# Performance work log

Hardware: AMD Instinct MI355X
Metric: run time of the kernel (lower is better)

## Reference

```python
import jax, jax.numpy as jnp
import numpy as np

HIDDEN = 256
ITEM_SIZE = 50000
SEQ_LEN = 256
BATCH = 256
ALPHA = 0.2      # LeakyReLU negative slope
LN_EPS = 1e-12


def setup_inputs() -> dict:
    key = jax.random.key(0)
    ks = jax.random.split(key, 8)
    item_seq = jax.random.randint(ks[0], (BATCH, SEQ_LEN), 0, ITEM_SIZE)
    item_emb_table = 0.02 * jax.random.normal(ks[1], (ITEM_SIZE, HIDDEN), dtype=jnp.float32)
    item_emb_table = item_emb_table.at[0].set(0.0)  # padding_idx=0
    pos_emb_table = 0.02 * jax.random.normal(ks[2], (SEQ_LEN, HIDDEN), dtype=jnp.float32)
    W = 0.02 * jax.random.normal(ks[3], (HIDDEN, HIDDEN), dtype=jnp.float32)  # stored [in,out]
    a1 = 0.02 * jax.random.normal(ks[4], (HIDDEN,), dtype=jnp.float32)  # a weight, first half (acts on h_i)
    a2 = 0.02 * jax.random.normal(ks[5], (HIDDEN,), dtype=jnp.float32)  # second half (acts on h_j)
    gamma = jnp.ones((HIDDEN,), dtype=jnp.float32)
    beta = jnp.zeros((HIDDEN,), dtype=jnp.float32)
    return {"item_seq": item_seq, "item_emb_table": item_emb_table,
            "pos_emb_table": pos_emb_table, "W": W, "a1": a1, "a2": a2,
            "gamma": gamma, "beta": beta}


def _layernorm(x, gamma, beta):
    mu = jnp.mean(x, axis=-1, keepdims=True)
    var = jnp.mean(jnp.square(x - mu), axis=-1, keepdims=True)
    return (x - mu) * jax.lax.rsqrt(var + LN_EPS) * gamma + beta


def reference(item_seq, item_emb_table, pos_emb_table, W, a1, a2, gamma, beta):
    B, L = item_seq.shape
    x = item_emb_table[item_seq] + pos_emb_table[jnp.arange(L)][None, :, :]  # [B,L,H]
    x = _layernorm(x, gamma, beta)
    # dropout is identity at eval time
    h = jnp.einsum('blh,hk->blk', x, W)  # GAT W projection, [B,L,H]
    # a([h_i ; h_j]) = a1.h_i + a2.h_j  -> rank-1 separable scores (same math, no O(L^2 H) concat)
    s1 = h @ a1  # [B,L]
    s2 = h @ a2  # [B,L]
    e = jax.nn.leaky_relu(s1[:, :, None] + s2[:, None, :], negative_slope=ALPHA)  # [B,L,L]
    # adj is all-ones, so the -9e15 mask is a no-op
    attn = jax.nn.softmax(e, axis=-1)
    return jnp.einsum('bij,bjh->bih', attn, h)  # [B,L,H]
```

## Files before the change

### kernel.cpp

```cpp
#include <hip/hip_runtime.h>
#include <hip/hip_bf16.h>

#define ALPHA  0.2f
#define L2E    1.4426950408889634f

typedef __attribute__((ext_vector_type(8))) short  short8;
typedef __attribute__((ext_vector_type(4))) float  f32x4;
typedef unsigned short u16;

__device__ __forceinline__ u16 f2bf(float f) {
    union { __hip_bfloat16 h; u16 u; } v;
    v.h = __float2bfloat16(f);
    return v.u;
}
__device__ __forceinline__ unsigned pk2(float a, float b) {
    union { __hip_bfloat162 h2; unsigned u; } v;
    float2 f2; f2.x = a; f2.y = b;
    v.h2 = __float22bfloat162_rn(f2);
    return v.u;
}
__device__ __forceinline__ float lrelu(float x) { return fmaxf(x, ALPHA * x); }

__global__ void prep(const float* __restrict__ W, const float* __restrict__ a1,
                     const float* __restrict__ a2, u16* __restrict__ wfrag,
                     float* __restrict__ w1, float* __restrict__ w2) {
    int b = blockIdx.x;
    if (b < 64) {
        int t    = threadIdx.x;
        int pair = b * 2 + (t >> 7);
        int l    = (t >> 1) & 63;
        int jh   = (t & 1) * 4;
        int ks   = pair >> 4, cb = pair & 15;
        int c  = cb * 16 + (l & 15);
        int k0 = ks * 32 + (l >> 4) * 8 + jh;
        ushort4 o;
        o.x = f2bf(W[(size_t)(k0 + 0) * 256 + c]);
        o.y = f2bf(W[(size_t)(k0 + 1) * 256 + c]);
        o.z = f2bf(W[(size_t)(k0 + 2) * 256 + c]);
        o.w = f2bf(W[(size_t)(k0 + 3) * 256 + c]);
        *(ushort4*)&wfrag[(size_t)pair * 512 + l * 8 + jh] = o;
    } else {
        int bb = b - 64;
        int wv = threadIdx.x >> 6, lane = threadIdx.x & 63;
        for (int kk = 0; kk < 16; ++kk) {
            int k = bb * 64 + wv * 16 + kk;
            float4 wv4 = *(const float4*)(W + (size_t)k * 256 + 4 * lane);
            float4 a14 = *(const float4*)(a1 + 4 * lane);
            float4 a24 = *(const float4*)(a2 + 4 * lane);
            float d1 = wv4.x*a14.x + wv4.y*a14.y + wv4.z*a14.z + wv4.w*a14.w;
            float d2 = wv4.x*a24.x + wv4.y*a24.y + wv4.z*a24.z + wv4.w*a24.w;
            #pragma unroll
            for (int off = 32; off; off >>= 1) {
                d1 += __shfl_xor(d1, off);
                d2 += __shfl_xor(d2, off);
            }
            if (lane == 0) { w1[k] = d1; w2[k] = d2; }
        }
    }
}

__global__ __launch_bounds__(1024)
void gat(const int* __restrict__ item_seq, const float* __restrict__ emb,
         const float* __restrict__ pos, const float* __restrict__ gamma,
         const float* __restrict__ beta, const float* __restrict__ w1,
         const float* __restrict__ w2, const u16* __restrict__ wfrag,
         float* __restrict__ out)
{
    __shared__ u16 xb[256 * 256];
    __shared__ __align__(16) float s1s[256], s2s[256], mS[256];
    __shared__ __align__(16) float part[256][4];
    __shared__ float wmax[16];
    const int b    = blockIdx.x;
    const int tid  = threadIdx.x;
    const int lane = tid & 63, wid = tid >> 6, g = lane >> 4, li = lane & 15;
    const int iw_  = wid >> 2, nw = wid & 3;

    {
        float4 g4  = *(const float4*)(gamma + 4 * lane);
        float4 b4  = *(const float4*)(beta  + 4 * lane);
        float4 w14 = *(const float4*)(w1    + 4 * lane);
        float4 w24 = *(const float4*)(w2    + 4 * lane);
        float4 u4, t4;
        u4.x = g4.x*w14.x; u4.y = g4.y*w14.y; u4.z = g4.z*w14.z; u4.w = g4.w*w14.w;
        t4.x = g4.x*w24.x; t4.y = g4.y*w24.y; t4.z = g4.z*w24.z; t4.w = g4.w*w24.w;
        float cA = u4.x + u4.y + u4.z + u4.w;
        float cB = t4.x + t4.y + t4.z + t4.w;
        float cC = b4.x*w14.x + b4.y*w14.y + b4.z*w14.z + b4.w*w14.w;
        float cD = b4.x*w24.x + b4.y*w24.y + b4.z*w24.z + b4.w*w24.w;
        #pragma unroll
        for (int off = 32; off; off >>= 1) {
            cA += __shfl_xor(cA, off); cB += __shfl_xor(cB, off);
            cC += __shfl_xor(cC, off); cD += __shfl_xor(cD, off);
        }
        float rm = -3.0e38f;
        #pragma unroll 2
        for (int it = 0; it < 8; ++it) {
            int rA = it * 32 + wid, rB = rA + 16;
            int gA = item_seq[b * 256 + rA];
            int gB = item_seq[b * 256 + rB];
            float4 eA = *(const float4*)(emb + (size_t)gA * 256 + 4 * lane);
            float4 pA = *(const float4*)(pos + (size_t)rA * 256 + 4 * lane);
            float4 eB = *(const float4*)(emb + (size_t)gB * 256 + 4 * lane);
            float4 pB = *(const float4*)(pos + (size_t)rB * 256 + 4 * lane);
            float4 vA, vB;
            vA.x = eA.x + pA.x; vA.y = eA.y + pA.y; vA.z = eA.z + pA.z; vA.w = eA.w + pA.w;
            vB.x = eB.x + pB.x; vB.y = eB.y + pB.y; vB.z = eB.z + pB.z; vB.w = eB.w + pB.w;
            float sa = vA.x + vA.y + vA.z + vA.w;
            float qa = vA.x*vA.x + vA.y*vA.y + vA.z*vA.z + vA.w*vA.w;
            float d1a = vA.x*u4.x + vA.y*u4.y + vA.z*u4.z + vA.w*u4.w;
            float d2a = vA.x*t4.x + vA.y*t4.y + vA.z*t4.z + vA.w*t4.w;
            float sb = vB.x + vB.y + vB.z + vB.w;
            float qb = vB.x*vB.x + vB.y*vB.y + vB.z*vB.z + vB.w*vB.w;
            float d1b = vB.x*u4.x + vB.y*u4.y + vB.z*u4.z + vB.w*u4.w;
            float d2b = vB.x*t4.x + vB.y*t4.y + vB.z*t4.z + vB.w*t4.w;
            #pragma unroll
            for (int off = 32; off; off >>= 1) {
                sa  += __shfl_xor(sa,  off);  sb  += __shfl_xor(sb,  off);
                qa  += __shfl_xor(qa,  off);  qb  += __shfl_xor(qb,  off);
                d1a += __shfl_xor(d1a, off);  d1b += __shfl_xor(d1b, off);
                d2a += __shfl_xor(d2a, off);  d2b += __shfl_xor(d2b, off);
            }
            float muA = sa * (1.0f/256.0f);
            float rsA = rsqrtf(qa * (1.0f/256.0f) - muA*muA + 1e-12f);
            float muB = sb * (1.0f/256.0f);
            float rsB = rsqrtf(qb * (1.0f/256.0f) - muB*muB + 1e-12f);
            float s1A = (rsA * (d1a - muA * cA) + cC) * L2E;
            float s2A = (rsA * (d2a - muA * cB) + cD) * L2E;
            float s1B = (rsB * (d1b - muB * cA) + cC) * L2E;
            float s2B = (rsB * (d2b - muB * cB) + cD) * L2E;
            if (lane == 0) {
                s1s[rA] = s1A; s2s[rA] = s2A;
                s1s[rB] = s1B; s2s[rB] = s2B;
            }
            rm = fmaxf(rm, fmaxf(s2A, s2B));
            uint2 oA, oB;
            oA.x = pk2((vA.x - muA) * rsA * g4.x + b4.x,
                       (vA.y - muA) * rsA * g4.y + b4.y);
            oA.y = pk2((vA.z - muA) * rsA * g4.z + b4.z,
                       (vA.w - muA) * rsA * g4.w + b4.w);
            oB.x = pk2((vB.x - muB) * rsB * g4.x + b4.x,
                       (vB.y - muB) * rsB * g4.y + b4.y);
            oB.y = pk2((vB.z - muB) * rsB * g4.z + b4.z,
                       (vB.w - muB) * rsB * g4.w + b4.w);
            int sl = (lane >> 1), sub = (lane & 1) * 4;
            *(uint2*)&xb[rA * 256 + ((sl ^ (rA & 7)) << 3) + sub] = oA;
            *(uint2*)&xb[rB * 256 + ((sl ^ (rB & 7)) << 3) + sub] = oB;
        }
        if (lane == 0) wmax[wid] = rm;
    }
    __syncthreads();

    {
        float s2m = wmax[0];
        #pragma unroll
        for (int k = 1; k < 16; ++k) s2m = fmaxf(s2m, wmax[k]);
        int i = tid >> 2, jq = tid & 3;
        float s1v = s1s[i];
        float mi  = lrelu(s1v + s2m);
        float aB0 = s1v - mi;
        float bB0 = ALPHA * s1v - mi;
        float sum = 0.f;
        const float4* sp = (const float4*)&s2s[jq * 64];
        #pragma unroll 4
        for (int j4 = 0; j4 < 16; ++j4) {
            float4 sv = sp[j4];
            sum += __builtin_amdgcn_exp2f(fmaxf(aB0 + sv.x, fmaf(ALPHA, sv.x, bB0)));
            sum += __builtin_amdgcn_exp2f(fmaxf(aB0 + sv.y, fmaf(ALPHA, sv.y, bB0)));
            sum += __builtin_amdgcn_exp2f(fmaxf(aB0 + sv.z, fmaf(ALPHA, sv.z, bB0)));
            sum += __builtin_amdgcn_exp2f(fmaxf(aB0 + sv.w, fmaf(ALPHA, sv.w, bB0)));
        }
        if (jq == 0) mS[i] = mi;
        part[i][jq] = sum;
    }

    f32x4 acc[4][4];
    #pragma unroll
    for (int mt = 0; mt < 4; ++mt)
        #pragma unroll
        for (int nt = 0; nt < 4; ++nt)
            acc[mt][nt] = (f32x4){0.f, 0.f, 0.f, 0.f};

    #pragma unroll
    for (int ks = 0; ks < 8; ++ks) {
        short8 bf[4];
        #pragma unroll
        for (int nt = 0; nt < 4; ++nt)
            bf[nt] = *(const short8*)(wfrag
                       + ((size_t)(ks * 16 + nw * 4 + nt) * 64 + lane) * 8);
        #pragma unroll
        for (int mt = 0; mt < 4; ++mt) {
            int rl = iw_ * 64 + mt * 16 + li;
            short8 af = *(const short8*)&xb[rl * 256 + (((ks*4+g) ^ (rl & 7)) << 3)];
            #pragma unroll
            for (int nt = 0; nt < 4; ++nt)
                acc[mt][nt] = __builtin_amdgcn_mfma_f32_16x16x32_bf16(
                    af, bf[nt], acc[mt][nt], 0, 0, 0);
        }
    }
    __syncthreads();

    #pragma unroll
    for (int mt = 0; mt < 4; ++mt)
        #pragma unroll
        for (int nt = 0; nt < 4; ++nt) {
            int c  = nw * 64 + nt * 16 + li;
            int i0 = iw_ * 64 + mt * 16 + 4 * g;
            uint2 o;
            o.x = pk2(acc[mt][nt][0], acc[mt][nt][1]);
            o.y = pk2(acc[mt][nt][2], acc[mt][nt][3]);
            *(uint2*)&xb[c * 256 + (((i0 >> 3) ^ (c & 7)) << 3) + (i0 & 7)] = o;
        }
    __syncthreads();

    {
        const int ig2 = wid >> 1;
        const int ng2 = wid & 1;
        f32x4 oacc[2][8];
        #pragma unroll
        for (int mt = 0; mt < 2; ++mt)
            #pragma unroll
            for (int nt = 0; nt < 8; ++nt)
                oacc[mt][nt] = (f32x4){0.f, 0.f, 0.f, 0.f};

        float aBase[2], bBase[2];
        #pragma unroll
        for (int mt = 0; mt < 2; ++mt) {
            int i = ig2 * 32 + mt * 16 + li;
            float lsum = part[i][0] + part[i][1] + part[i][2] + part[i][3];
            float Mi = mS[i] + __log2f(lsum);
            float s1v = s1s[i];
            aBase[mt] = s1v - Mi;
            bBase[mt] = ALPHA * s1v - Mi;
        }

        #pragma unroll
        for (int js = 0; js < 8; ++js) {
            float4 sv0 = *(const float4*)&s2s[js * 32 + g * 8];
            float4 sv1 = *(const float4*)&s2s[js * 32 + g * 8 + 4];
            float s2l[8] = {sv0.x, sv0.y, sv0.z, sv0.w, sv1.x, sv1.y, sv1.z, sv1.w};

            short8 pfr[2];
            #pragma unroll
            for (int mt = 0; mt < 2; ++mt) {
                union { unsigned int u[4]; short8 s; } pk;
                #pragma unroll
                for (int q2 = 0; q2 < 4; ++q2) {
                    float sA = s2l[2 * q2], sB = s2l[2 * q2 + 1];
                    float p0 = __builtin_amdgcn_exp2f(
                        fmaxf(aBase[mt] + sA, fmaf(ALPHA, sA, bBase[mt])));
                    float p1 = __builtin_amdgcn_exp2f(
                        fmaxf(aBase[mt] + sB, fmaf(ALPHA, sB, bBase[mt])));
                    pk.u[q2] = pk2(p0, p1);
                }
                pfr[mt] = pk.s;
            }
            #pragma unroll
            for (int nt = 0; nt < 8; ++nt) {
                int cl = ng2 * 128 + nt * 16 + li;
                short8 vf = *(const short8*)&xb[cl * 256
                              + (((js * 4 + g) ^ (cl & 7)) << 3)];
                #pragma unroll
                for (int mt = 0; mt < 2; ++mt)
                    oacc[mt][nt] = __builtin_amdgcn_mfma_f32_16x16x32_bf16(
                        pfr[mt], vf, oacc[mt][nt], 0, 0, 0);
            }
        }

        size_t ob = (size_t)b * (256 * 256);
        #pragma unroll
        for (int mt = 0; mt < 2; ++mt)
            #pragma unroll
            for (int nt = 0; nt < 8; ++nt) {
                int c  = ng2 * 128 + nt * 16 + li;
                int i0 = ig2 * 32 + mt * 16 + 4 * g;
                #pragma unroll
                for (int q2 = 0; q2 < 4; ++q2)
                    out[ob + (size_t)(i0 + q2) * 256 + c] = oacc[mt][nt][q2];
            }
    }
}

extern "C" void kernel_launch(void* const* d_in, const int* in_sizes, int n_in,
                              void* d_out, int out_size, void* d_ws, size_t ws_size,
                              hipStream_t stream) {
    (void)in_sizes; (void)n_in; (void)out_size; (void)ws_size;
    const int*   seq   = (const int*)d_in[0];
    const float* emb   = (const float*)d_in[1];
    const float* pos   = (const float*)d_in[2];
    const float* W     = (const float*)d_in[3];
    const float* a1    = (const float*)d_in[4];
    const float* a2    = (const float*)d_in[5];
    const float* gamma = (const float*)d_in[6];
    const float* beta  = (const float*)d_in[7];

    char* ws = (char*)d_ws;
    u16*   wfrag = (u16*)ws;
    float* w1    = (float*)(ws + 131072);
    float* w2    = (float*)(ws + 132096);

    hipLaunchKernelGGL(prep, dim3(68), dim3(256), 0, stream, W, a1, a2, wfrag, w1, w2);
    hipLaunchKernelGGL(gat, dim3(256), dim3(1024), 0, stream,
                       seq, emb, pos, gamma, beta, w1, w2, wfrag, (float*)d_out);
}
```

Baseline: 59.25 us.

## Fuse softmax denominator into PV pass and prefetch W fragments

Removes the separate softmax row-sum pass, which computed the exp sums up front, and instead accumulates row sums from the same exp values used to build the P fragments. The output is normalized at the end with a reciprocal gathered through shuffles. The LayerNorm load loop now handles four rows per iteration to raise memory-level parallelism, and the W fragment loads in the projection GEMM are software-prefetched one k-step ahead. The risk is that sums are taken in fp32 before bf16 rounding of P, so they differ slightly from the packed values, and that register pressure rises.

```diff
diff --git a/kernel.cpp b/kernel.cpp
--- a/kernel.cpp
+++ b/kernel.cpp
@@ -67,9 +67,9 @@
          float* __restrict__ out)
 {
     __shared__ u16 xb[256 * 256];
-    __shared__ __align__(16) float s1s[256], s2s[256], mS[256];
-    __shared__ __align__(16) float part[256][4];
+    __shared__ __align__(16) float s1s[256], s2s[256];
     __shared__ float wmax[16];
+    __shared__ float s2r;
     const int b    = blockIdx.x;
     const int tid  = threadIdx.x;
     const int lane = tid & 63, wid = tid >> 6, g = lane >> 4, li = lane & 15;
@@ -93,84 +93,67 @@
             cC += __shfl_xor(cC, off); cD += __shfl_xor(cD, off);
         }
         float rm = -3.0e38f;
-        #pragma unroll 2
-        for (int it = 0; it < 8; ++it) {
-            int rA = it * 32 + wid, rB = rA + 16;
-            int gA = item_seq[b * 256 + rA];
-            int gB = item_seq[b * 256 + rB];
-            float4 eA = *(const float4*)(emb + (size_t)gA * 256 + 4 * lane);
-            float4 pA = *(const float4*)(pos + (size_t)rA * 256 + 4 * lane);
-            float4 eB = *(const float4*)(emb + (size_t)gB * 256 + 4 * lane);
-            float4 pB = *(const float4*)(pos + (size_t)rB * 256 + 4 * lane);
-            float4 vA, vB;
-            vA.x = eA.x + pA.x; vA.y = eA.y + pA.y; vA.z = eA.z + pA.z; vA.w = eA.w + pA.w;
-            vB.x = eB.x + pB.x; vB.y = eB.y + pB.y; vB.z = eB.z + pB.z; vB.w = eB.w + pB.w;
-            float sa = vA.x + vA.y + vA.z + vA.w;
-            float qa = vA.x*vA.x + vA.y*vA.y + vA.z*vA.z + vA.w*vA.w;
-            float d1a = vA.x*u4.x + vA.y*u4.y + vA.z*u4.z + vA.w*u4.w;
-            float d2a = vA.x*t4.x + vA.y*t4.y + vA.z*t4.z + vA.w*t4.w;
-            float sb = vB.x + vB.y + vB.z + vB.w;
-            float qb = vB.x*vB.x + vB.y*vB.y + vB.z*vB.z + vB.w*vB.w;
-            float d1b = vB.x*u4.x + vB.y*u4.y + vB.z*u4.z + vB.w*u4.w;
-            float d2b = vB.x*t4.x + vB.y*t4.y + vB.z*t4.z + vB.w*t4.w;
+        for (int it = 0; it < 4; ++it) {
+            int r0 = it * 64 + wid;
+            int gI[4];
+            #pragma unroll
+            for (int m = 0; m < 4; ++m) gI[m] = item_seq[b * 256 + r0 + m * 16];
+            float4 e[4], p[4];
+            #pragma unroll
+            for (int m = 0; m < 4; ++m)
+                e[m] = *(const float4*)(emb + (size_t)gI[m] * 256 + 4 * lane);
+            #pragma unroll
+            for (int m = 0; m < 4; ++m)
+                p[m] = *(const float4*)(pos + (size_t)(r0 + m * 16) * 256 + 4 * lane);
+            float4 v[4]; float s[4], q[4], d1[4], d2[4];
+            #pragma unroll
+            for (int m = 0; m < 4; ++m) {
+                float4 vv;
+                vv.x = e[m].x + p[m].x; vv.y = e[m].y + p[m].y;
+                vv.z = e[m].z + p[m].z; vv.w = e[m].w + p[m].w;
+                v[m] = vv;
+                s[m]  = vv.x + vv.y + vv.z + vv.w;
+                q[m]  = vv.x*vv.x + vv.y*vv.y + vv.z*vv.z + vv.w*vv.w;
+                d1[m] = vv.x*u4.x + vv.y*u4.y + vv.z*u4.z + vv.w*u4.w;
+                d2[m] = vv.x*t4.x + vv.y*t4.y + vv.z*t4.z + vv.w*t4.w;
+            }
             #pragma unroll
             for (int off = 32; off; off >>= 1) {
-                sa  += __shfl_xor(sa,  off);  sb  += __shfl_xor(sb,  off);
-                qa  += __shfl_xor(qa,  off);  qb  += __shfl_xor(qb,  off);
-                d1a += __shfl_xor(d1a, off);  d1b += __shfl_xor(d1b, off);
-                d2a += __shfl_xor(d2a, off);  d2b += __shfl_xor(d2b, off);
-            }
-            float muA = sa * (1.0f/256.0f);
-            float rsA = rsqrtf(qa * (1.0f/256.0f) - muA*muA + 1e-12f);
-            float muB = sb * (1.0f/256.0f);
-            float rsB = rsqrtf(qb * (1.0f/256.0f) - muB*muB + 1e-12f);
-            float s1A = (rsA * (d1a - muA * cA) + cC) * L2E;
-            float s2A = (rsA * (d2a - muA * cB) + cD) * L2E;
-            float s1B = (rsB * (d1b - muB * cA) + cC) * L2E;
-            float s2B = (rsB * (d2b - muB * cB) + cD) * L2E;
-            if (lane == 0) {
-                s1s[rA] = s1A; s2s[rA] = s2A;
-                s1s[rB] = s1B; s2s[rB] = s2B;
-            }
-            rm = fmaxf(rm, fmaxf(s2A, s2B));
-            uint2 oA, oB;
-            oA.x = pk2((vA.x - muA) * rsA * g4.x + b4.x,
-                       (vA.y - muA) * rsA * g4.y + b4.y);
-            oA.y = pk2((vA.z - muA) * rsA * g4.z + b4.z,
-                       (vA.w - muA) * rsA * g4.w + b4.w);
-            oB.x = pk2((vB.x - muB) * rsB * g4.x + b4.x,
-                       (vB.y - muB) * rsB * g4.y + b4.y);
-            oB.y = pk2((vB.z - muB) * rsB * g4.z + b4.z,
-                       (vB.w - muB) * rsB * g4.w + b4.w);
-            int sl = (lane >> 1), sub = (lane & 1) * 4;
-            *(uint2*)&xb[rA * 256 + ((sl ^ (rA & 7)) << 3) + sub] = oA;
-            *(uint2*)&xb[rB * 256 + ((sl ^ (rB & 7)) << 3) + sub] = oB;
+                #pragma unroll
+                for (int m = 0; m < 4; ++m) {
+                    s[m]  += __shfl_xor(s[m],  off);
+                    q[m]  += __shfl_xor(q[m],  off);
+                    d1[m] += __shfl_xor(d1[m], off);
+                    d2[m] += __shfl_xor(d2[m], off);
+                }
+            }
+            #pragma unroll
+            for (int m = 0; m < 4; ++m) {
+                int r = r0 + m * 16;
+                float mu  = s[m] * (1.0f/256.0f);
+                float rs  = rsqrtf(q[m] * (1.0f/256.0f) - mu*mu + 1e-12f);
+                float s1v = (rs * (d1[m] - mu * cA) + cC) * L2E;
+                float s2v = (rs * (d2[m] - mu * cB) + cD) * L2E;
+                if (lane == 0) { s1s[r] = s1v; s2s[r] = s2v; }
+                rm = fmaxf(rm, s2v);
+                uint2 o;
+                o.x = pk2((v[m].x - mu) * rs * g4.x + b4.x,
+                          (v[m].y - mu) * rs * g4.y + b4.y);
+                o.y = pk2((v[m].z - mu) * rs * g4.z + b4.z,
+                          (v[m].w - mu) * rs * g4.w + b4.w);
+                int sl = (lane >> 1), sub = (lane & 1) * 4;
+                *(uint2*)&xb[r * 256 + ((sl ^ (r & 7)) << 3) + sub] = o;
+            }
         }
         if (lane == 0) wmax[wid] = rm;
     }
     __syncthreads();
 
-    {
-        float s2m = wmax[0];
-        #pragma unroll
-        for (int k = 1; k < 16; ++k) s2m = fmaxf(s2m, wmax[k]);
-        int i = tid >> 2, jq = tid & 3;
-        float s1v = s1s[i];
-        float mi  = lrelu(s1v + s2m);
-        float aB0 = s1v - mi;
-        float bB0 = ALPHA * s1v - mi;
-        float sum = 0.f;
-        const float4* sp = (const float4*)&s2s[jq * 64];
-        #pragma unroll 4
-        for (int j4 = 0; j4 < 16; ++j4) {
-            float4 sv = sp[j4];
-            sum += __builtin_amdgcn_exp2f(fmaxf(aB0 + sv.x, fmaf(ALPHA, sv.x, bB0)));
-            sum += __builtin_amdgcn_exp2f(fmaxf(aB0 + sv.y, fmaf(ALPHA, sv.y, bB0)));
-            sum += __builtin_amdgcn_exp2f(fmaxf(aB0 + sv.z, fmaf(ALPHA, sv.z, bB0)));
-            sum += __builtin_amdgcn_exp2f(fmaxf(aB0 + sv.w, fmaf(ALPHA, sv.w, bB0)));
-        }
-        if (jq == 0) mS[i] = mi;
-        part[i][jq] = sum;
+    if (tid == 0) {
+        float m0 = wmax[0];
+        #pragma unroll
+        for (int k = 1; k < 16; ++k) m0 = fmaxf(m0, wmax[k]);
+        s2r = m0;
     }
 
     f32x4 acc[4][4];
@@ -180,21 +163,34 @@
         for (int nt = 0; nt < 4; ++nt)
             acc[mt][nt] = (f32x4){0.f, 0.f, 0.f, 0.f};
 
-    #pragma unroll
-    for (int ks = 0; ks < 8; ++ks) {
+    {
         short8 bf[4];
         #pragma unroll
         for (int nt = 0; nt < 4; ++nt)
             bf[nt] = *(const short8*)(wfrag
-                       + ((size_t)(ks * 16 + nw * 4 + nt) * 64 + lane) * 8);
-        #pragma unroll
-        for (int mt = 0; mt < 4; ++mt) {
-            int rl = iw_ * 64 + mt * 16 + li;
-            short8 af = *(const short8*)&xb[rl * 256 + (((ks*4+g) ^ (rl & 7)) << 3)];
-            #pragma unroll
-            for (int nt = 0; nt < 4; ++nt)
-                acc[mt][nt] = __builtin_amdgcn_mfma_f32_16x16x32_bf16(
-                    af, bf[nt], acc[mt][nt], 0, 0, 0);
+                       + ((size_t)(nw * 4 + nt) * 64 + lane) * 8);
+        #pragma unroll
+        for (int ks = 0; ks < 8; ++ks) {
+            short8 bfn[4];
+            if (ks < 7) {
+                #pragma unroll
+                for (int nt = 0; nt < 4; ++nt)
+                    bfn[nt] = *(const short8*)(wfrag
+                               + ((size_t)((ks + 1) * 16 + nw * 4 + nt) * 64 + lane) * 8);
+            }
+            #pragma unroll
+            for (int mt = 0; mt < 4; ++mt) {
+                int rl = iw_ * 64 + mt * 16 + li;
+                short8 af = *(const short8*)&xb[rl * 256 + (((ks*4+g) ^ (rl & 7)) << 3)];
+                #pragma unroll
+                for (int nt = 0; nt < 4; ++nt)
+                    acc[mt][nt] = __builtin_amdgcn_mfma_f32_16x16x32_bf16(
+                        af, bf[nt], acc[mt][nt], 0, 0, 0);
+            }
+            if (ks < 7) {
+                #pragma unroll
+                for (int nt = 0; nt < 4; ++nt) bf[nt] = bfn[nt];
+            }
         }
     }
     __syncthreads();
@@ -222,15 +218,16 @@
             for (int nt = 0; nt < 8; ++nt)
                 oacc[mt][nt] = (f32x4){0.f, 0.f, 0.f, 0.f};
 
-        float aBase[2], bBase[2];
+        float s2m = s2r;
+        float aBase[2], bBase[2], pl[2];
         #pragma unroll
         for (int mt = 0; mt < 2; ++mt) {
             int i = ig2 * 32 + mt * 16 + li;
-            float lsum = part[i][0] + part[i][1] + part[i][2] + part[i][3];
-            float Mi = mS[i] + __log2f(lsum);
             float s1v = s1s[i];
-            aBase[mt] = s1v - Mi;
-            bBase[mt] = ALPHA * s1v - Mi;
+            float mi  = lrelu(s1v + s2m);
+            aBase[mt] = s1v - mi;
+            bBase[mt] = fmaf(ALPHA, s1v, -mi);
+            pl[mt] = 0.f;
         }
 
         #pragma unroll
@@ -250,6 +247,7 @@
                         fmaxf(aBase[mt] + sA, fmaf(ALPHA, sA, bBase[mt])));
                     float p1 = __builtin_amdgcn_exp2f(
                         fmaxf(aBase[mt] + sB, fmaf(ALPHA, sB, bBase[mt])));
+                    pl[mt] += p0 + p1;
                     pk.u[q2] = pk2(p0, p1);
                 }
                 pfr[mt] = pk.s;
@@ -266,6 +264,17 @@
             }
         }
 
+        float linv[2][4];
+        #pragma unroll
+        for (int mt = 0; mt < 2; ++mt) {
+            float t = pl[mt];
+            t += __shfl_xor(t, 16);
+            t += __shfl_xor(t, 32);
+            #pragma unroll
+            for (int q2 = 0; q2 < 4; ++q2)
+                linv[mt][q2] = 1.0f / __shfl(t, 4 * g + q2);
+        }
+
         size_t ob = (size_t)b * (256 * 256);
         #pragma unroll
         for (int mt = 0; mt < 2; ++mt)
@@ -275,7 +284,7 @@
                 int i0 = ig2 * 32 + mt * 16 + 4 * g;
                 #pragma unroll
                 for (int q2 = 0; q2 < 4; ++q2)
-                    out[ob + (size_t)(i0 + q2) * 256 + c] = oacc[mt][nt][q2];
+                    out[ob + (size_t)(i0 + q2) * 256 + c] = oacc[mt][nt][q2] * linv[mt][q2];
             }
     }
 }
```

Measured after the change: 59.91 us. Within noise of the previous version (+1.1%).

## Split LN+projection into halves and fold softmax normalization into epilogue

Applied to the files above, without the earlier changes.

The embedding, LayerNorm and projection work is split into two 128-row halves. Gathers for the second half are issued early and the first-half MFMA projection runs while that second half is being prepared, which is meant to hide gather latency behind tensor-core work. The separate softmax row-sum pass (with its part/mS shared arrays and log) is removed. Row sums are instead accumulated during the P computation, and the output is scaled by their reciprocal in the epilogue. The wave tiling of the projection also changes from 4x4 to 2x8. The trade-off is more live registers (eU, acc0, acc1), which raises spill or pressure risk at 1024 threads.

```diff
diff --git a/kernel.cpp b/kernel.cpp
--- a/kernel.cpp
+++ b/kernel.cpp
@@ -67,152 +67,220 @@
          float* __restrict__ out)
 {
     __shared__ u16 xb[256 * 256];
-    __shared__ __align__(16) float s1s[256], s2s[256], mS[256];
-    __shared__ __align__(16) float part[256][4];
+    __shared__ __align__(16) float s1s[256], s2s[256];
     __shared__ float wmax[16];
     const int b    = blockIdx.x;
     const int tid  = threadIdx.x;
     const int lane = tid & 63, wid = tid >> 6, g = lane >> 4, li = lane & 15;
-    const int iw_  = wid >> 2, nw = wid & 3;
-
-    {
-        float4 g4  = *(const float4*)(gamma + 4 * lane);
-        float4 b4  = *(const float4*)(beta  + 4 * lane);
-        float4 w14 = *(const float4*)(w1    + 4 * lane);
-        float4 w24 = *(const float4*)(w2    + 4 * lane);
-        float4 u4, t4;
-        u4.x = g4.x*w14.x; u4.y = g4.y*w14.y; u4.z = g4.z*w14.z; u4.w = g4.w*w14.w;
-        t4.x = g4.x*w24.x; t4.y = g4.y*w24.y; t4.z = g4.z*w24.z; t4.w = g4.w*w24.w;
-        float cA = u4.x + u4.y + u4.z + u4.w;
-        float cB = t4.x + t4.y + t4.z + t4.w;
-        float cC = b4.x*w14.x + b4.y*w14.y + b4.z*w14.z + b4.w*w14.w;
-        float cD = b4.x*w24.x + b4.y*w24.y + b4.z*w24.z + b4.w*w24.w;
+    const int iw2  = wid >> 3, nw8 = wid & 7;
+
+    float4 g4  = *(const float4*)(gamma + 4 * lane);
+    float4 b4  = *(const float4*)(beta  + 4 * lane);
+    float4 w14 = *(const float4*)(w1    + 4 * lane);
+    float4 w24 = *(const float4*)(w2    + 4 * lane);
+    float4 u4, t4;
+    u4.x = g4.x*w14.x; u4.y = g4.y*w14.y; u4.z = g4.z*w14.z; u4.w = g4.w*w14.w;
+    t4.x = g4.x*w24.x; t4.y = g4.y*w24.y; t4.z = g4.z*w24.z; t4.w = g4.w*w24.w;
+    float cA = u4.x + u4.y + u4.z + u4.w;
+    float cB = t4.x + t4.y + t4.z + t4.w;
+    float cC = b4.x*w14.x + b4.y*w14.y + b4.z*w14.z + b4.w*w14.w;
+    float cD = b4.x*w24.x + b4.y*w24.y + b4.z*w24.z + b4.w*w24.w;
+    #pragma unroll
+    for (int off = 32; off; off >>= 1) {
+        cA += __shfl_xor(cA, off); cB += __shfl_xor(cB, off);
+        cC += __shfl_xor(cC, off); cD += __shfl_xor(cD, off);
+    }
+
+    int gU[8];
+    #pragma unroll
+    for (int m = 0; m < 8; ++m) gU[m] = item_seq[b * 256 + 128 + m * 16 + wid];
+
+    float rm = -3.0e38f;
+
+    #pragma unroll 2
+    for (int it = 0; it < 4; ++it) {
+        int rA = it * 32 + wid, rB = rA + 16;
+        int gA = item_seq[b * 256 + rA];
+        int gB = item_seq[b * 256 + rB];
+        float4 eA = *(const float4*)(emb + (size_t)gA * 256 + 4 * lane);
+        float4 pA = *(const float4*)(pos + (size_t)rA * 256 + 4 * lane);
+        float4 eB = *(const float4*)(emb + (size_t)gB * 256 + 4 * lane);
+        float4 pB = *(const float4*)(pos + (size_t)rB * 256 + 4 * lane);
+        float4 vA, vB;
+        vA.x = eA.x + pA.x; vA.y = eA.y + pA.y; vA.z = eA.z + pA.z; vA.w = eA.w + pA.w;
+        vB.x = eB.x + pB.x; vB.y = eB.y + pB.y; vB.z = eB.z + pB.z; vB.w = eB.w + pB.w;
+        float sa = vA.x + vA.y + vA.z + vA.w;
+        float qa = vA.x*vA.x + vA.y*vA.y + vA.z*vA.z + vA.w*vA.w;
+        float d1a = vA.x*u4.x + vA.y*u4.y + vA.z*u4.z + vA.w*u4.w;
+        float d2a = vA.x*t4.x + vA.y*t4.y + vA.z*t4.z + vA.w*t4.w;
+        float sb = vB.x + vB.y + vB.z + vB.w;
+        float qb = vB.x*vB.x + vB.y*vB.y + vB.z*vB.z + vB.w*vB.w;
+        float d1b = vB.x*u4.x + vB.y*u4.y + vB.z*u4.z + vB.w*u4.w;
+        float d2b = vB.x*t4.x + vB.y*t4.y + vB.z*t4.z + vB.w*t4.w;
         #pragma unroll
         for (int off = 32; off; off >>= 1) {
-            cA += __shfl_xor(cA, off); cB += __shfl_xor(cB, off);
-            cC += __shfl_xor(cC, off); cD += __shfl_xor(cD, off);
-        }
-        float rm = -3.0e38f;
-        #pragma unroll 2
-        for (int it = 0; it < 8; ++it) {
-            int rA = it * 32 + wid, rB = rA + 16;
-            int gA = item_seq[b * 256 + rA];
-            int gB = item_seq[b * 256 + rB];
-            float4 eA = *(const float4*)(emb + (size_t)gA * 256 + 4 * lane);
-            float4 pA = *(const float4*)(pos + (size_t)rA * 256 + 4 * lane);
-            float4 eB = *(const float4*)(emb + (size_t)gB * 256 + 4 * lane);
-            float4 pB = *(const float4*)(pos + (size_t)rB * 256 + 4 * lane);
-            float4 vA, vB;
-            vA.x = eA.x + pA.x; vA.y = eA.y + pA.y; vA.z = eA.z + pA.z; vA.w = eA.w + pA.w;
-            vB.x = eB.x + pB.x; vB.y = eB.y + pB.y; vB.z = eB.z + pB.z; vB.w = eB.w + pB.w;
-            float sa = vA.x + vA.y + vA.z + vA.w;
-            float qa = vA.x*vA.x + vA.y*vA.y + vA.z*vA.z + vA.w*vA.w;
-            float d1a = vA.x*u4.x + vA.y*u4.y + vA.z*u4.z + vA.w*u4.w;
-            float d2a = vA.x*t4.x + vA.y*t4.y + vA.z*t4.z + vA.w*t4.w;
-            float sb = vB.x + vB.y + vB.z + vB.w;
-            float qb = vB.x*vB.x + vB.y*vB.y + vB.z*vB.z + vB.w*vB.w;
-            float d1b = vB.x*u4.x + vB.y*u4.y + vB.z*u4.z + vB.w*u4.w;
-            float d2b = vB.x*t4.x + vB.y*t4.y + vB.z*t4.z + vB.w*t4.w;
-            #pragma unroll
-            for (int off = 32; off; off >>= 1) {
-                sa  += __shfl_xor(sa,  off);  sb  += __shfl_xor(sb,  off);
-                qa  += __shfl_xor(qa,  off);  qb  += __shfl_xor(qb,  off);
-                d1a += __shfl_xor(d1a, off);  d1b += __shfl_xor(d1b, off);
-                d2a += __shfl_xor(d2a, off);  d2b += __shfl_xor(d2b, off);
-            }
-            float muA = sa * (1.0f/256.0f);
-            float rsA = rsqrtf(qa * (1.0f/256.0f) - muA*muA + 1e-12f);
-            float muB = sb * (1.0f/256.0f);
-            float rsB = rsqrtf(qb * (1.0f/256.0f) - muB*muB + 1e-12f);
-            float s1A = (rsA * (d1a - muA * cA) + cC) * L2E;
-            float s2A = (rsA * (d2a - muA * cB) + cD) * L2E;
-            float s1B = (rsB * (d1b - muB * cA) + cC) * L2E;
-            float s2B = (rsB * (d2b - muB * cB) + cD) * L2E;
-            if (lane == 0) {
-                s1s[rA] = s1A; s2s[rA] = s2A;
-                s1s[rB] = s1B; s2s[rB] = s2B;
-            }
-            rm = fmaxf(rm, fmaxf(s2A, s2B));
-            uint2 oA, oB;
-            oA.x = pk2((vA.x - muA) * rsA * g4.x + b4.x,
-                       (vA.y - muA) * rsA * g4.y + b4.y);
-            oA.y = pk2((vA.z - muA) * rsA * g4.z + b4.z,
-                       (vA.w - muA) * rsA * g4.w + b4.w);
-            oB.x = pk2((vB.x - muB) * rsB * g4.x + b4.x,
-                       (vB.y - muB) * rsB * g4.y + b4.y);
-            oB.y = pk2((vB.z - muB) * rsB * g4.z + b4.z,
-                       (vB.w - muB) * rsB * g4.w + b4.w);
-            int sl = (lane >> 1), sub = (lane & 1) * 4;
-            *(uint2*)&xb[rA * 256 + ((sl ^ (rA & 7)) << 3) + sub] = oA;
-            *(uint2*)&xb[rB * 256 + ((sl ^ (rB & 7)) << 3) + sub] = oB;
-        }
-        if (lane == 0) wmax[wid] = rm;
-    }
+            sa  += __shfl_xor(sa,  off);  sb  += __shfl_xor(sb,  off);
+            qa  += __shfl_xor(qa,  off);  qb  += __shfl_xor(qb,  off);
+            d1a += __shfl_xor(d1a, off);  d1b += __shfl_xor(d1b, off);
+            d2a += __shfl_xor(d2a, off);  d2b += __shfl_xor(d2b, off);
+        }
+        float muA = sa * (1.0f/256.0f);
+        float rsA = rsqrtf(qa * (1.0f/256.0f) - muA*muA + 1e-12f);
+        float muB = sb * (1.0f/256.0f);
+        float rsB = rsqrtf(qb * (1.0f/256.0f) - muB*muB + 1e-12f);
+        float s1A = (rsA * (d1a - muA * cA) + cC) * L2E;
+        float s2A = (rsA * (d2a - muA * cB) + cD) * L2E;
+        float s1B = (rsB * (d1b - muB * cA) + cC) * L2E;
+        float s2B = (rsB * (d2b - muB * cB) + cD) * L2E;
+        if (lane == 0) {
+            s1s[rA] = s1A; s2s[rA] = s2A;
+            s1s[rB] = s1B; s2s[rB] = s2B;
+        }
+        rm = fmaxf(rm, fmaxf(s2A, s2B));
+        uint2 oA, oB;
+        oA.x = pk2((vA.x - muA) * rsA * g4.x + b4.x,
+                   (vA.y - muA) * rsA * g4.y + b4.y);
+        oA.y = pk2((vA.z - muA) * rsA * g4.z + b4.z,
+                   (vA.w - muA) * rsA * g4.w + b4.w);
+        oB.x = pk2((vB.x - muB) * rsB * g4.x + b4.x,
+                   (vB.y - muB) * rsB * g4.y + b4.y);
+        oB.y = pk2((vB.z - muB) * rsB * g4.z + b4.z,
+                   (vB.w - muB) * rsB * g4.w + b4.w);
+        int sl = (lane >> 1), sub = (lane & 1) * 4;
+        *(uint2*)&xb[rA * 256 + ((sl ^ (rA & 7)) << 3) + sub] = oA;
+        *(uint2*)&xb[rB * 256 + ((sl ^ (rB & 7)) << 3) + sub] = oB;
+    }
+    __syncthreads();
+
+    float4 eU[8];
+    #pragma unroll
+    for (int m = 0; m < 8; ++m)
+        eU[m] = *(const float4*)(emb + (size_t)gU[m] * 256 + 4 * lane);
+
+    f32x4 acc0[4][2];
+    #pragma unroll
+    for (int mt = 0; mt < 4; ++mt)
+        #pragma unroll
+        for (int nt = 0; nt < 2; ++nt)
+            acc0[mt][nt] = (f32x4){0.f, 0.f, 0.f, 0.f};
+    #pragma unroll
+    for (int ks = 0; ks < 8; ++ks) {
+        short8 bf[2];
+        #pragma unroll
+        for (int nt = 0; nt < 2; ++nt)
+            bf[nt] = *(const short8*)(wfrag
+                       + ((size_t)(ks * 16 + nw8 * 2 + nt) * 64 + lane) * 8);
+        #pragma unroll
+        for (int mt = 0; mt < 4; ++mt) {
+            int rl = iw2 * 64 + mt * 16 + li;
+            short8 af = *(const short8*)&xb[rl * 256 + (((ks*4+g) ^ (rl & 7)) << 3)];
+            #pragma unroll
+            for (int nt = 0; nt < 2; ++nt)
+                acc0[mt][nt] = __builtin_amdgcn_mfma_f32_16x16x32_bf16(
+                    af, bf[nt], acc0[mt][nt], 0, 0, 0);
+        }
+    }
+
+    #pragma unroll 2
+    for (int it = 0; it < 4; ++it) {
+        int rA = 128 + it * 32 + wid, rB = rA + 16;
+        float4 eA = eU[2 * it], eB = eU[2 * it + 1];
+        float4 pA = *(const float4*)(pos + (size_t)rA * 256 + 4 * lane);
+        float4 pB = *(const float4*)(pos + (size_t)rB * 256 + 4 * lane);
+        float4 vA, vB;
+        vA.x = eA.x + pA.x; vA.y = eA.y + pA.y; vA.z = eA.z + pA.z; vA.w = eA.w + pA.w;
+        vB.x = eB.x + pB.x; vB.y = eB.y + pB.y; vB.z = eB.z + pB.z; vB.w = eB.w + pB.w;
+        float sa = vA.x + vA.y + vA.z + vA.w;
+        float qa = vA.x*vA.x + vA.y*vA.y + vA.z*vA.z + vA.w*vA.w;
+        float d1a = vA.x*u4.x + vA.y*u4.y + vA.z*u4.z + vA.w*u4.w;
+        float d2a = vA.x*t4.x + vA.y*t4.y + vA.z*t4.z + vA.w*t4.w;
+        float sb = vB.x + vB.y + vB.z + vB.w;
+        float qb = vB.x*vB.x + vB.y*vB.y + vB.z*vB.z + vB.w*vB.w;
+        float d1b = vB.x*u4.x + vB.y*u4.y + vB.z*u4.z + vB.w*u4.w;
+        float d2b = vB.x*t4.x + vB.y*t4.y + vB.z*t4.z + vB.w*t4.w;
+        #pragma unroll
+        for (int off = 32; off; off >>= 1) {
+            sa  += __shfl_xor(sa,  off);  sb  += __shfl_xor(sb,  off);
+            qa  += __shfl_xor(qa,  off);  qb  += __shfl_xor(qb,  off);
+            d1a += __shfl_xor(d1a, off);  d1b += __shfl_xor(d1b, off);
+            d2a += __shfl_xor(d2a, off);  d2b += __shfl_xor(d2b, off);
+        }
+        float muA = sa * (1.0f/256.0f);
+        float rsA = rsqrtf(qa * (1.0f/256.0f) - muA*muA + 1e-12f);
+        float muB = sb * (1.0f/256.0f);
+        float rsB = rsqrtf(qb * (1.0f/256.0f) - muB*muB + 1e-12f);
+        float s1A = (rsA * (d1a - muA * cA) + cC) * L2E;
+        float s2A = (rsA * (d2a - muA * cB) + cD) * L2E;
+        float s1B = (rsB * (d1b - muB * cA) + cC) * L2E;
+        float s2B = (rsB * (d2b - muB * cB) + cD) * L2E;
+        if (lane == 0) {
+            s1s[rA] = s1A; s2s[rA] = s2A;
+            s1s[rB] = s1B; s2s[rB] = s2B;
+        }
+        rm = fmaxf(rm, fmaxf(s2A, s2B));
+        uint2 oA, oB;
+        oA.x = pk2((vA.x - muA) * rsA * g4.x + b4.x,
+                   (vA.y - muA) * rsA * g4.y + b4.y);
+        oA.y = pk2((vA.z - muA) * rsA * g4.z + b4.z,
+                   (vA.w - muA) * rsA * g4.w + b4.w);
+        oB.x = pk2((vB.x - muB) * rsB * g4.x + b4.x,
+                   (vB.y - muB) * rsB * g4.y + b4.y);
+        oB.y = pk2((vB.z - muB) * rsB * g4.z + b4.z,
+                   (vB.w - muB) * rsB * g4.w + b4.w);
+        int sl = (lane >> 1), sub = (lane & 1) * 4;
+        *(uint2*)&xb[rA * 256 + ((sl ^ (rA & 7)) << 3) + sub] = oA;
+        *(uint2*)&xb[rB * 256 + ((sl ^ (rB & 7)) << 3) + sub] = oB;
+    }
+    if (lane == 0) wmax[wid] = rm;
+    __syncthreads();
+
+    f32x4 acc1[4][2];
+    #pragma unroll
+    for (int mt = 0; mt < 4; ++mt)
+        #pragma unroll
+        for (int nt = 0; nt < 2; ++nt)
+            acc1[mt][nt] = (f32x4){0.f, 0.f, 0.f, 0.f};
+    #pragma unroll
+    for (int ks = 0; ks < 8; ++ks) {
+        short8 bf[2];
+        #pragma unroll
+        for (int nt = 0; nt < 2; ++nt)
+            bf[nt] = *(const short8*)(wfrag
+                       + ((size_t)(ks * 16 + nw8 * 2 + nt) * 64 + lane) * 8);
+        #pragma unroll
+        for (int mt = 0; mt < 4; ++mt) {
+            int rl = 128 + iw2 * 64 + mt * 16 + li;
+            short8 af = *(const short8*)&xb[rl * 256 + (((ks*4+g) ^ (rl & 7)) << 3)];
+            #pragma unroll
+            for (int nt = 0; nt < 2; ++nt)
+                acc1[mt][nt] = __builtin_amdgcn_mfma_f32_16x16x32_bf16(
+                    af, bf[nt], acc1[mt][nt], 0, 0, 0);
+        }
+    }
+    __syncthreads();
+
+    #pragma unroll
+    for (int mt = 0; mt < 4; ++mt)
+        #pragma unroll
+        for (int nt = 0; nt < 2; ++nt) {
+            int c  = nw8 * 32 + nt * 16 + li;
+            int j0 = iw2 * 64 + mt * 16 + 4 * g;
+            uint2 o0, o1;
+            o0.x = pk2(acc0[mt][nt][0], acc0[mt][nt][1]);
+            o0.y = pk2(acc0[mt][nt][2], acc0[mt][nt][3]);
+            o1.x = pk2(acc1[mt][nt][0], acc1[mt][nt][1]);
+            o1.y = pk2(acc1[mt][nt][2], acc1[mt][nt][3]);
+            *(uint2*)&xb[c * 256 + (((j0 >> 3) ^ (c & 7)) << 3) + (j0 & 7)] = o0;
+            int j1 = j0 + 128;
+            *(uint2*)&xb[c * 256 + (((j1 >> 3) ^ (c & 7)) << 3) + (j1 & 7)] = o1;
+        }
     __syncthreads();
 
     {
         float s2m = wmax[0];
         #pragma unroll
         for (int k = 1; k < 16; ++k) s2m = fmaxf(s2m, wmax[k]);
-        int i = tid >> 2, jq = tid & 3;
-        float s1v = s1s[i];
-        float mi  = lrelu(s1v + s2m);
-        float aB0 = s1v - mi;
-        float bB0 = ALPHA * s1v - mi;
-        float sum = 0.f;
-        const float4* sp = (const float4*)&s2s[jq * 64];
-        #pragma unroll 4
-        for (int j4 = 0; j4 < 16; ++j4) {
-            float4 sv = sp[j4];
-            sum += __builtin_amdgcn_exp2f(fmaxf(aB0 + sv.x, fmaf(ALPHA, sv.x, bB0)));
-            sum += __builtin_amdgcn_exp2f(fmaxf(aB0 + sv.y, fmaf(ALPHA, sv.y, bB0)));
-            sum += __builtin_amdgcn_exp2f(fmaxf(aB0 + sv.z, fmaf(ALPHA, sv.z, bB0)));
-            sum += __builtin_amdgcn_exp2f(fmaxf(aB0 + sv.w, fmaf(ALPHA, sv.w, bB0)));
-        }
-        if (jq == 0) mS[i] = mi;
-        part[i][jq] = sum;
-    }
-
-    f32x4 acc[4][4];
-    #pragma unroll
-    for (int mt = 0; mt < 4; ++mt)
-        #pragma unroll
-        for (int nt = 0; nt < 4; ++nt)
-            acc[mt][nt] = (f32x4){0.f, 0.f, 0.f, 0.f};
-
-    #pragma unroll
-    for (int ks = 0; ks < 8; ++ks) {
-        short8 bf[4];
-        #pragma unroll
-        for (int nt = 0; nt < 4; ++nt)
-            bf[nt] = *(const short8*)(wfrag
-                       + ((size_t)(ks * 16 + nw * 4 + nt) * 64 + lane) * 8);
-        #pragma unroll
-        for (int mt = 0; mt < 4; ++mt) {
-            int rl = iw_ * 64 + mt * 16 + li;
-            short8 af = *(const short8*)&xb[rl * 256 + (((ks*4+g) ^ (rl & 7)) << 3)];
-            #pragma unroll
-            for (int nt = 0; nt < 4; ++nt)
-                acc[mt][nt] = __builtin_amdgcn_mfma_f32_16x16x32_bf16(
-                    af, bf[nt], acc[mt][nt], 0, 0, 0);
-        }
-    }
-    __syncthreads();
-
-    #pragma unroll
-    for (int mt = 0; mt < 4; ++mt)
-        #pragma unroll
-        for (int nt = 0; nt < 4; ++nt) {
-            int c  = nw * 64 + nt * 16 + li;
-            int i0 = iw_ * 64 + mt * 16 + 4 * g;
-            uint2 o;
-            o.x = pk2(acc[mt][nt][0], acc[mt][nt][1]);
-            o.y = pk2(acc[mt][nt][2], acc[mt][nt][3]);
-            *(uint2*)&xb[c * 256 + (((i0 >> 3) ^ (c & 7)) << 3) + (i0 & 7)] = o;
-        }
-    __syncthreads();
-
-    {
+
         const int ig2 = wid >> 1;
         const int ng2 = wid & 1;
         f32x4 oacc[2][8];
@@ -222,15 +290,15 @@
             for (int nt = 0; nt < 8; ++nt)
                 oacc[mt][nt] = (f32x4){0.f, 0.f, 0.f, 0.f};
 
-        float aBase[2], bBase[2];
+        float aBase[2], bBase[2], pl[2];
         #pragma unroll
         for (int mt = 0; mt < 2; ++mt) {
             int i = ig2 * 32 + mt * 16 + li;
-            float lsum = part[i][0] + part[i][1] + part[i][2] + part[i][3];
-            float Mi = mS[i] + __log2f(lsum);
             float s1v = s1s[i];
-            aBase[mt] = s1v - Mi;
-            bBase[mt] = ALPHA * s1v - Mi;
+            float mi  = lrelu(s1v + s2m);
+            aBase[mt] = s1v - mi;
+            bBase[mt] = fmaf(ALPHA, s1v, -mi);
+            pl[mt] = 0.f;
         }
 
         #pragma unroll
@@ -250,6 +318,7 @@
                         fmaxf(aBase[mt] + sA, fmaf(ALPHA, sA, bBase[mt])));
                     float p1 = __builtin_amdgcn_exp2f(
                         fmaxf(aBase[mt] + sB, fmaf(ALPHA, sB, bBase[mt])));
+                    pl[mt] += p0 + p1;
                     pk.u[q2] = pk2(p0, p1);
                 }
                 pfr[mt] = pk.s;
@@ -266,6 +335,17 @@
             }
         }
 
+        float linv[2][4];
+        #pragma unroll
+        for (int mt = 0; mt < 2; ++mt) {
+            float t = pl[mt];
+            t += __shfl_xor(t, 16);
+            t += __shfl_xor(t, 32);
+            #pragma unroll
+            for (int q2 = 0; q2 < 4; ++q2)
+                linv[mt][q2] = 1.0f / __shfl(t, 4 * g + q2);
+        }
+
         size_t ob = (size_t)b * (256 * 256);
         #pragma unroll
         for (int mt = 0; mt < 2; ++mt)
@@ -275,7 +355,7 @@
                 int i0 = ig2 * 32 + mt * 16 + 4 * g;
                 #pragma unroll
                 for (int q2 = 0; q2 < 4; ++q2)
-                    out[ob + (size_t)(i0 + q2) * 256 + c] = oacc[mt][nt][q2];
+                    out[ob + (size_t)(i0 + q2) * 256 + c] = oacc[mt][nt][q2] * linv[mt][q2];
             }
     }
 }
```

Measured after the change: 72.57 us. 22.5% more time.
